# Kernel tuning notes

Measured on AMD Instinct MI355X. Metric: run time of the kernel, lower is better.

The kernel has to match this reference:

```python
import jax, jax.numpy as jnp
import numpy as np

N, E, IN, H, D = 50000, 800000, 128, 2, 64  # nodes, edges, in_dim, heads, out_dim per head
EPS = 1e-16  # PyG softmax denominator epsilon


def setup_inputs() -> dict:
    key = jax.random.key(0)
    ks = jax.random.split(key, 10)
    s = 1.0 / np.sqrt(IN)
    u = lambda k, shape: jax.random.uniform(k, shape, jnp.float32, -s, s)
    return {
        "x": jax.random.normal(ks[0], (N, IN), jnp.float32),
        "edge_index": jax.random.randint(ks[1], (2, E), 0, N, jnp.int64),
        "Wq": u(ks[2], (IN, H * D)), "bq": u(ks[3], (H * D,)),
        "Wk": u(ks[4], (IN, H * D)), "bk": u(ks[5], (H * D,)),
        "Wv": u(ks[6], (IN, H * D)), "bv": u(ks[7], (H * D,)),
        "Ws": u(ks[8], (IN, H * D)), "bs": u(ks[9], (H * D,)),
    }


def reference(x, edge_index, Wq, bq, Wk, bk, Wv, bv, Ws, bs):
    src, dst = edge_index[0], edge_index[1]
    # node-level projections [N, H, D]
    q = (x @ Wq + bq).reshape(N, H, D)
    k = (x @ Wk + bk).reshape(N, H, D)
    v = (x @ Wv + bv).reshape(N, H, D)
    # per-edge attention logits [E, H]
    alpha = jnp.einsum('ehd,ehd->eh', q[dst], k[src]) / np.float32(np.sqrt(D))
    # segment softmax over incoming edges of each dst node
    amax = jax.ops.segment_max(alpha, dst, num_segments=N)      # [N, H]
    amax = jnp.where(jnp.isfinite(amax), amax, 0.0)
    ealpha = jnp.exp(alpha - amax[dst])                          # [E, H]
    denom = jax.ops.segment_sum(ealpha, dst, num_segments=N)     # [N, H]
    w = ealpha / (denom[dst] + EPS)                              # [E, H]
    # scatter-aggregate weighted values -> [N, H, D]
    agg = jax.ops.segment_sum(w[:, :, None] * v[src], dst, num_segments=N)
    out = agg.reshape(N, H * D) + (x @ Ws + bs)                  # root/skip term
    return jax.nn.relu(out)
```

## Files before the change

kernel.cpp:

```cpp
#include <hip/hip_runtime.h>
#include <hip/hip_bf16.h>


#define N_NODES 50000
#define E_EDGES 800000
#define IN_DIM  128
#define HD      128
#define NPB     256
#define NB      196
#define EB      2048
#define NBLK_AC ((E_EDGES + EB - 1) / EB)
#define NTILES  ((N_NODES + 63) / 64)
#define PBLK    256
#define PSCALE  0.18033688011112042f

typedef float  f32x4  __attribute__((ext_vector_type(4)));
typedef float  f32x2  __attribute__((ext_vector_type(2)));
typedef __bf16 bf16x8 __attribute__((ext_vector_type(8)));
typedef unsigned short u16x8 __attribute__((ext_vector_type(8)));

__device__ __forceinline__ float bf2f(unsigned short u) {
    return __uint_as_float((unsigned int)u << 16);
}

__global__ __launch_bounds__(512) void proj_kernel(
    const float* __restrict__ x,
    const float* __restrict__ Wq, const float* __restrict__ bq,
    const float* __restrict__ Wk, const float* __restrict__ bk,
    const float* __restrict__ Wv, const float* __restrict__ bv,
    const float* __restrict__ Ws, const float* __restrict__ bs,
    __bf16* __restrict__ qb, unsigned char* __restrict__ kv8,
    __bf16* __restrict__ sbuf)
{
    __shared__ __bf16 xs[64][136];

    const int tid  = threadIdx.x;
    const int lane = tid & 63;
    const int wave = tid >> 6;
    const int l15  = lane & 15;
    const int g    = lane >> 4;

    const int p    = wave >> 1;
    const int colh = (wave & 1) * 64;
    const float* Wp     = (p == 0) ? Wq : (p == 1) ? Wk : (p == 2) ? Wv : Ws;
    const float* bias_p = (p == 0) ? bq : (p == 1) ? bk : (p == 2) ? bv : bs;

    bf16x8 Bf[4][4];
    #pragma unroll
    for (int ks = 0; ks < 4; ++ks) {
        #pragma unroll
        for (int cf = 0; cf < 4; ++cf) {
            bf16x8 b;
            #pragma unroll
            for (int j = 0; j < 8; ++j)
                b[j] = (__bf16)Wp[(size_t)(ks * 32 + g * 8 + j) * HD + colh + cf * 16 + l15];
            Bf[ks][cf] = b;
        }
    }

    float bias_v[4];
    #pragma unroll
    for (int cf = 0; cf < 4; ++cf) bias_v[cf] = bias_p[colh + cf * 16 + l15];

    const int srow = tid >> 5;
    const int sc4  = tid & 31;

    int t = blockIdx.x;
    float4 pre[4];
    if (t < NTILES) {
        #pragma unroll
        for (int it = 0; it < 4; ++it) {
            int row  = it * 16 + srow;
            int grow = t * 64 + row;
            pre[it] = (grow < N_NODES) ? *(const float4*)(x + (size_t)grow * IN_DIM + sc4 * 4)
                                       : make_float4(0.f, 0.f, 0.f, 0.f);
        }
    }

    for (; t < NTILES; t += PBLK) {
        __syncthreads();
        #pragma unroll
        for (int it = 0; it < 4; ++it) {
            int row = it * 16 + srow;
            __bf16* dst = &xs[row][sc4 * 4];
            dst[0] = (__bf16)pre[it].x; dst[1] = (__bf16)pre[it].y;
            dst[2] = (__bf16)pre[it].z; dst[3] = (__bf16)pre[it].w;
        }
        __syncthreads();

        int tn = t + PBLK;
        if (tn < NTILES) {
            #pragma unroll
            for (int it = 0; it < 4; ++it) {
                int row  = it * 16 + srow;
                int grow = tn * 64 + row;
                pre[it] = (grow < N_NODES) ? *(const float4*)(x + (size_t)grow * IN_DIM + sc4 * 4)
                                           : make_float4(0.f, 0.f, 0.f, 0.f);
            }
        }

        f32x4 acc[4][4];
        #pragma unroll
        for (int i = 0; i < 4; ++i)
            #pragma unroll
            for (int j = 0; j < 4; ++j) acc[i][j] = (f32x4){0.f, 0.f, 0.f, 0.f};

        #pragma unroll
        for (int ks = 0; ks < 4; ++ks) {
            #pragma unroll
            for (int rf = 0; rf < 4; ++rf) {
                bf16x8 A = *(const bf16x8*)&xs[rf * 16 + l15][ks * 32 + g * 8];
                #pragma unroll
                for (int cf = 0; cf < 4; ++cf)
                    acc[rf][cf] = __builtin_amdgcn_mfma_f32_16x16x32_bf16(A, Bf[ks][cf], acc[rf][cf], 0, 0, 0);
            }
        }

        const int nodebase = t * 64;
        if (p == 0 || p == 3) {
            __bf16* outp = (p == 0) ? qb : sbuf;
            #pragma unroll
            for (int cf = 0; cf < 4; ++cf) {
                int col = colh + cf * 16 + l15;
                #pragma unroll
                for (int rf = 0; rf < 4; ++rf) {
                    #pragma unroll
                    for (int r = 0; r < 4; ++r) {
                        int grow = nodebase + rf * 16 + g * 4 + r;
                        if (grow < N_NODES)
                            outp[(size_t)grow * HD + col] = (__bf16)(acc[rf][cf][r] + bias_v[cf]);
                    }
                }
            }
        } else {
            unsigned char* outp = kv8 + ((p == 2) ? 128 : 0);
            #pragma unroll
            for (int cf = 0; cf < 4; ++cf) {
                int col = colh + cf * 16 + l15;
                #pragma unroll
                for (int rf = 0; rf < 4; ++rf) {
                    #pragma unroll
                    for (int r = 0; r < 4; ++r) {
                        int grow = nodebase + rf * 16 + g * 4 + r;
                        if (grow < N_NODES) {
                            float val = acc[rf][cf][r] + bias_v[cf];
                            unsigned int pk = __builtin_amdgcn_cvt_pk_fp8_f32(val, val, 0, false);
                            outp[(size_t)grow * 256 + col] = (unsigned char)(pk & 0xff);
                        }
                    }
                }
            }
        }
    }
}

__global__ __launch_bounds__(256) void histA(
    const int* __restrict__ ei, int* __restrict__ hist)
{
    __shared__ int h[NB];
    const int tid = threadIdx.x;
    for (int i = tid; i < NB; i += 256) h[i] = 0;
    __syncthreads();

    const int* dsts = ei + E_EDGES;
    const int base = blockIdx.x * EB;
    #pragma unroll
    for (int half = 0; half < 2; ++half) {
        int e0 = base + half * 1024 + tid * 4;
        if (e0 + 3 < E_EDGES) {
            int4 d = *(const int4*)(dsts + e0);
            atomicAdd(&h[d.x >> 8], 1);
            atomicAdd(&h[d.y >> 8], 1);
            atomicAdd(&h[d.z >> 8], 1);
            atomicAdd(&h[d.w >> 8], 1);
        } else {
            for (int j = 0; j < 4; ++j)
                if (e0 + j < E_EDGES) atomicAdd(&h[dsts[e0 + j] >> 8], 1);
        }
    }
    __syncthreads();
    for (int i = tid; i < NB; i += 256)
        hist[i * NBLK_AC + blockIdx.x] = h[i];
}

__global__ __launch_bounds__(256) void scanB1(
    int* __restrict__ hist, int* __restrict__ sums)
{
    __shared__ int a[512];
    const int tid = threadIdx.x;
    const int b   = blockIdx.x;
    int* hb = hist + (size_t)b * NBLK_AC;

    a[tid]       = (tid       < NBLK_AC) ? hb[tid]       : 0;
    a[tid + 256] = (tid + 256 < NBLK_AC) ? hb[tid + 256] : 0;
    __syncthreads();
    #pragma unroll
    for (int d = 1; d < 512; d <<= 1) {
        int v0 = a[tid],       u0 = (tid       >= d) ? a[tid - d]       : 0;
        int v1 = a[tid + 256], u1 = (tid + 256 >= d) ? a[tid + 256 - d] : 0;
        __syncthreads();
        a[tid] = v0 + u0; a[tid + 256] = v1 + u1;
        __syncthreads();
    }
    if (tid < NBLK_AC)       hb[tid]       = (tid == 0) ? 0 : a[tid - 1];
    if (tid + 256 < NBLK_AC) hb[tid + 256] = a[tid + 255];
    if (tid == 0) sums[b] = a[NBLK_AC - 1];
}

__global__ __launch_bounds__(256) void scanB2(
    const int* __restrict__ sums, int* __restrict__ binbase)
{
    __shared__ int a[256];
    const int tid = threadIdx.x;
    a[tid] = (tid < NB) ? sums[tid] : 0;
    __syncthreads();
    #pragma unroll
    for (int d = 1; d < 256; d <<= 1) {
        int v = a[tid];
        int u = (tid >= d) ? a[tid - d] : 0;
        __syncthreads();
        a[tid] = v + u;
        __syncthreads();
    }
    if (tid < NB) binbase[tid] = (tid == 0) ? 0 : a[tid - 1];
    if (tid == 0) binbase[NB] = a[NB - 1] + 0;
    if (tid == 0) binbase[NB] = a[255];
}

__global__ __launch_bounds__(256) void scatterC(
    const int* __restrict__ ei, const int* __restrict__ hist,
    const int* __restrict__ binbase, int2* __restrict__ part)
{
    __shared__ int hb[NB];
    __shared__ int h2[NB];
    const int tid = threadIdx.x;
    for (int i = tid; i < NB; i += 256) {
        hb[i] = hist[i * NBLK_AC + blockIdx.x] + binbase[i];
        h2[i] = 0;
    }
    __syncthreads();

    const int* srcs = ei;
    const int* dsts = ei + E_EDGES;
    const int base = blockIdx.x * EB;
    #pragma unroll
    for (int half = 0; half < 2; ++half) {
        int e0 = base + half * 1024 + tid * 4;
        if (e0 + 3 < E_EDGES) {
            int4 s4 = *(const int4*)(srcs + e0);
            int4 d4 = *(const int4*)(dsts + e0);
            int bin, r;
            bin = d4.x >> 8; r = atomicAdd(&h2[bin], 1); part[hb[bin] + r] = make_int2(s4.x, d4.x);
            bin = d4.y >> 8; r = atomicAdd(&h2[bin], 1); part[hb[bin] + r] = make_int2(s4.y, d4.y);
            bin = d4.z >> 8; r = atomicAdd(&h2[bin], 1); part[hb[bin] + r] = make_int2(s4.z, d4.z);
            bin = d4.w >> 8; r = atomicAdd(&h2[bin], 1); part[hb[bin] + r] = make_int2(s4.w, d4.w);
        } else {
            for (int j = 0; j < 4; ++j) {
                if (e0 + j < E_EDGES) {
                    int sv = srcs[e0 + j], dv = dsts[e0 + j];
                    int bin = dv >> 8;
                    int r = atomicAdd(&h2[bin], 1);
                    part[hb[bin] + r] = make_int2(sv, dv);
                }
            }
        }
    }
}

__global__ __launch_bounds__(256) void buildD(
    const int2* __restrict__ part, const int* __restrict__ binbase,
    int* __restrict__ slot, int* __restrict__ nbase)
{
    __shared__ int cnt2[NPB];
    __shared__ int pfx[NPB];
    __shared__ int ofs[NPB];
    const int tid = threadIdx.x;
    const int b   = blockIdx.x;
    const int lo  = binbase[b];
    const int hi  = binbase[b + 1];
    const int n0  = b * NPB;

    cnt2[tid] = 0;
    __syncthreads();
    for (int i = lo + tid; i < hi; i += 256)
        atomicAdd(&cnt2[part[i].y - n0], 1);
    __syncthreads();

    pfx[tid] = cnt2[tid];
    __syncthreads();
    #pragma unroll
    for (int d = 1; d < NPB; d <<= 1) {
        int v = pfx[tid];
        int u = (tid >= d) ? pfx[tid - d] : 0;
        __syncthreads();
        pfx[tid] = v + u;
        __syncthreads();
    }
    const int excl = pfx[tid] - cnt2[tid];
    ofs[tid] = excl;
    const int node = n0 + tid;
    if (node < N_NODES) nbase[node] = lo + excl;
    if (b == NB - 1 && tid == 0) nbase[N_NODES] = E_EDGES;
    __syncthreads();

    for (int i = lo + tid; i < hi; i += 256) {
        int2 e = part[i];
        int r = atomicAdd(&ofs[e.y - n0], 1);
        slot[lo + r] = e.x;
    }
}

__global__ __launch_bounds__(256) void aggregate_kernel(
    const __bf16* __restrict__ qb, const unsigned char* __restrict__ kv8,
    const __bf16* __restrict__ sbuf,
    const int* __restrict__ nbase, const int* __restrict__ slot,
    float* __restrict__ out)
{
    const int tid  = threadIdx.x;
    const int lane = tid & 63;
    const int wave = tid >> 6;
    const int h    = lane >> 5;
    const int lh   = lane & 31;
    const int s    = lh >> 4;
    const int l16  = lh & 15;
    const int node = blockIdx.x * 8 + wave * 2 + h;
    const bool nvalid = node < N_NODES;
    const int nc = nvalid ? node : 0;

    const int bse = nbase[nc];
    const int deg = nvalid ? (nbase[nc + 1] - bse) : 0;

    u16x8 qu = *(const u16x8*)(qb + (size_t)nc * HD + 8 * l16);
    float qf[8];
    #pragma unroll
    for (int c = 0; c < 8; ++c) qf[c] = bf2f(qu[c]);

    int my_src = (lh < deg) ? slot[bse + lh] : 0;

    float lsum = 0.f;
    float acc[8];
    #pragma unroll
    for (int c = 0; c < 8; ++c) acc[c] = 0.f;

    const int sbase = h * 32;
    for (int i = 0; i < deg; i += 8) {
        int  jj[4], se[4];
        uint2 kr[4], vr[4];
        float d[4];

        #pragma unroll
        for (int r = 0; r < 4; ++r) {
            jj[r] = i + 2 * r + s;
            int sv = __shfl(my_src, sbase + (jj[r] & 31), 64);
            if (jj[r] >= 32) sv = slot[bse + jj[r]];
            se[r] = (jj[r] < deg) ? sv : 0;
        }
        #pragma unroll
        for (int r = 0; r < 4; ++r) {
            const unsigned char* rowp = kv8 + (size_t)se[r] * 256 + 8 * l16;
            kr[r] = *(const uint2*)rowp;
            vr[r] = *(const uint2*)(rowp + 128);
        }
        #pragma unroll
        for (int r = 0; r < 4; ++r) {
            f32x2 ka = __builtin_amdgcn_cvt_pk_f32_fp8(kr[r].x, 0);
            f32x2 kb_ = __builtin_amdgcn_cvt_pk_f32_fp8(kr[r].x, 1);
            f32x2 kc = __builtin_amdgcn_cvt_pk_f32_fp8(kr[r].y, 0);
            f32x2 kd = __builtin_amdgcn_cvt_pk_f32_fp8(kr[r].y, 1);
            d[r] = qf[0] * ka.x + qf[1] * ka.y + qf[2] * kb_.x + qf[3] * kb_.y
                 + qf[4] * kc.x + qf[5] * kc.y + qf[6] * kd.x + qf[7] * kd.y;
        }
        #pragma unroll
        for (int m = 1; m <= 4; m <<= 1) {
            d[0] += __shfl_xor(d[0], m);
            d[1] += __shfl_xor(d[1], m);
            d[2] += __shfl_xor(d[2], m);
            d[3] += __shfl_xor(d[3], m);
        }
        #pragma unroll
        for (int r = 0; r < 4; ++r) {
            float a2 = (jj[r] < deg) ? d[r] * PSCALE : -INFINITY;
            float p  = exp2f(a2);
            lsum += p;
            f32x2 va = __builtin_amdgcn_cvt_pk_f32_fp8(vr[r].x, 0);
            f32x2 vb_ = __builtin_amdgcn_cvt_pk_f32_fp8(vr[r].x, 1);
            f32x2 vc = __builtin_amdgcn_cvt_pk_f32_fp8(vr[r].y, 0);
            f32x2 vd = __builtin_amdgcn_cvt_pk_f32_fp8(vr[r].y, 1);
            acc[0] += p * va.x;  acc[1] += p * va.y;
            acc[2] += p * vb_.x; acc[3] += p * vb_.y;
            acc[4] += p * vc.x;  acc[5] += p * vc.y;
            acc[6] += p * vd.x;  acc[7] += p * vd.y;
        }
    }

    lsum += __shfl_xor(lsum, 16);
    #pragma unroll
    for (int c = 0; c < 8; ++c) acc[c] += __shfl_xor(acc[c], 16);

    float inv = (deg > 0) ? 1.f / (lsum + 1e-16f) : 0.f;
    u16x8 su = *(const u16x8*)(sbuf + (size_t)nc * HD + 8 * l16);

    f32x4 ov;
    #pragma unroll
    for (int cc = 0; cc < 4; ++cc) {
        float av;
        unsigned short sv;
        switch (cc) {
            case 0: av = s ? acc[4] : acc[0]; sv = s ? su[4] : su[0]; break;
            case 1: av = s ? acc[5] : acc[1]; sv = s ? su[5] : su[1]; break;
            case 2: av = s ? acc[6] : acc[2]; sv = s ? su[6] : su[2]; break;
            default: av = s ? acc[7] : acc[3]; sv = s ? su[7] : su[3]; break;
        }
        ov[cc] = fmaxf(av * inv + bf2f(sv), 0.f);
    }
    if (nvalid)
        *(f32x4*)(out + (size_t)node * HD + 8 * l16 + 4 * s) = ov;
}

extern "C" void kernel_launch(void* const* d_in, const int* in_sizes, int n_in,
                              void* d_out, int out_size, void* d_ws, size_t ws_size,
                              hipStream_t stream)
{
    const float* x  = (const float*)d_in[0];
    const int*   ei = (const int*)d_in[1];
    const float* Wq = (const float*)d_in[2];
    const float* bq = (const float*)d_in[3];
    const float* Wk = (const float*)d_in[4];
    const float* bk = (const float*)d_in[5];
    const float* Wv = (const float*)d_in[6];
    const float* bv = (const float*)d_in[7];
    const float* Ws = (const float*)d_in[8];
    const float* bs = (const float*)d_in[9];

    char* ws = (char*)d_ws;
    size_t off = 0;
    auto alloc = [&](size_t bytes) {
        void* p = ws + off;
        off += (bytes + 255) & ~(size_t)255;
        return p;
    };
    const size_t projB = (size_t)N_NODES * HD * sizeof(__bf16);
    __bf16* qb = (__bf16*)alloc(projB);
    unsigned char* kv8 = (unsigned char*)alloc((size_t)N_NODES * 256);
    __bf16* sbf = (__bf16*)alloc(projB);
    int* hist    = (int*)alloc((size_t)NB * NBLK_AC * sizeof(int));
    int* sums    = (int*)alloc((size_t)NB * sizeof(int));
    int* binbase = (int*)alloc((size_t)(NB + 1) * sizeof(int));
    int2* part   = (int2*)alloc((size_t)E_EDGES * sizeof(int2));
    int* slot    = (int*)alloc((size_t)E_EDGES * sizeof(int));
    int* nbase   = (int*)alloc((size_t)(N_NODES + 1) * sizeof(int));

    histA<<<NBLK_AC, 256, 0, stream>>>(ei, hist);
    scanB1<<<NB, 256, 0, stream>>>(hist, sums);
    scanB2<<<1, 256, 0, stream>>>(sums, binbase);
    scatterC<<<NBLK_AC, 256, 0, stream>>>(ei, hist, binbase, part);
    buildD<<<NB, 256, 0, stream>>>(part, binbase, slot, nbase);

    proj_kernel<<<PBLK, 512, 0, stream>>>(
        x, Wq, bq, Wk, bk, Wv, bv, Ws, bs, qb, kv8, sbf);

    aggregate_kernel<<<(N_NODES + 7) / 8, 256, 0, stream>>>(
        qb, kv8, sbf, nbase, slot, (float*)d_out);
}
```

Measured before the change: 91.97 us.

## Fuse partition kernels into one cooperative kernel and widen aggregate unroll

Merges the five CSR-building kernels (histogram, two scans, scatter, per-bin build) into a single cooperative launch that uses grid-wide syncs between phases, so four kernel launches and their gaps go away. The aggregate loop now processes 16 edges per iteration instead of 8, putting more gathers in flight. The projection grid is doubled from 256 to 512 blocks. The trade-offs are grid.sync overhead, the requirement that all 391 blocks be co-resident, and higher register pressure in the aggregate kernel.

```diff
diff --git a/kernel.cpp b/kernel.cpp
--- a/kernel.cpp
+++ b/kernel.cpp
@@ -1,5 +1,6 @@
 #include <hip/hip_runtime.h>
 #include <hip/hip_bf16.h>
+#include <hip/hip_cooperative_groups.h>
 
 
 #define N_NODES 50000
@@ -11,7 +12,7 @@
 #define EB      2048
 #define NBLK_AC ((E_EDGES + EB - 1) / EB)
 #define NTILES  ((N_NODES + 63) / 64)
-#define PBLK    256
+#define PBLK    512
 #define PSCALE  0.18033688011112042f
 
 typedef float  f32x4  __attribute__((ext_vector_type(4)));
@@ -154,159 +155,145 @@
     }
 }
 
-__global__ __launch_bounds__(256) void histA(
-    const int* __restrict__ ei, int* __restrict__ hist)
+__global__ __launch_bounds__(256) void partition_coop(
+    const int* __restrict__ ei, int* __restrict__ hist, int* __restrict__ sums,
+    int* __restrict__ binbase, int2* __restrict__ part,
+    int* __restrict__ slot, int* __restrict__ nbase)
 {
-    __shared__ int h[NB];
+    namespace cg = cooperative_groups;
+    cg::grid_group grid = cg::this_grid();
+    __shared__ int sh[768];
     const int tid = threadIdx.x;
-    for (int i = tid; i < NB; i += 256) h[i] = 0;
+    const int blk = blockIdx.x;
+    const int base = blk * EB;
+    const int* srcs = ei;
+    const int* dsts = ei + E_EDGES;
+
+    for (int i = tid; i < NB; i += 256) sh[i] = 0;
     __syncthreads();
-
-    const int* dsts = ei + E_EDGES;
-    const int base = blockIdx.x * EB;
     #pragma unroll
     for (int half = 0; half < 2; ++half) {
         int e0 = base + half * 1024 + tid * 4;
         if (e0 + 3 < E_EDGES) {
             int4 d = *(const int4*)(dsts + e0);
-            atomicAdd(&h[d.x >> 8], 1);
-            atomicAdd(&h[d.y >> 8], 1);
-            atomicAdd(&h[d.z >> 8], 1);
-            atomicAdd(&h[d.w >> 8], 1);
+            atomicAdd(&sh[d.x >> 8], 1);
+            atomicAdd(&sh[d.y >> 8], 1);
+            atomicAdd(&sh[d.z >> 8], 1);
+            atomicAdd(&sh[d.w >> 8], 1);
         } else {
             for (int j = 0; j < 4; ++j)
-                if (e0 + j < E_EDGES) atomicAdd(&h[dsts[e0 + j] >> 8], 1);
+                if (e0 + j < E_EDGES) atomicAdd(&sh[dsts[e0 + j] >> 8], 1);
         }
     }
     __syncthreads();
     for (int i = tid; i < NB; i += 256)
-        hist[i * NBLK_AC + blockIdx.x] = h[i];
-}
-
-__global__ __launch_bounds__(256) void scanB1(
-    int* __restrict__ hist, int* __restrict__ sums)
-{
-    __shared__ int a[512];
-    const int tid = threadIdx.x;
-    const int b   = blockIdx.x;
-    int* hb = hist + (size_t)b * NBLK_AC;
-
-    a[tid]       = (tid       < NBLK_AC) ? hb[tid]       : 0;
-    a[tid + 256] = (tid + 256 < NBLK_AC) ? hb[tid + 256] : 0;
-    __syncthreads();
-    #pragma unroll
-    for (int d = 1; d < 512; d <<= 1) {
-        int v0 = a[tid],       u0 = (tid       >= d) ? a[tid - d]       : 0;
-        int v1 = a[tid + 256], u1 = (tid + 256 >= d) ? a[tid + 256 - d] : 0;
-        __syncthreads();
-        a[tid] = v0 + u0; a[tid + 256] = v1 + u1;
-        __syncthreads();
-    }
-    if (tid < NBLK_AC)       hb[tid]       = (tid == 0) ? 0 : a[tid - 1];
-    if (tid + 256 < NBLK_AC) hb[tid + 256] = a[tid + 255];
-    if (tid == 0) sums[b] = a[NBLK_AC - 1];
-}
-
-__global__ __launch_bounds__(256) void scanB2(
-    const int* __restrict__ sums, int* __restrict__ binbase)
-{
-    __shared__ int a[256];
-    const int tid = threadIdx.x;
-    a[tid] = (tid < NB) ? sums[tid] : 0;
-    __syncthreads();
-    #pragma unroll
-    for (int d = 1; d < 256; d <<= 1) {
-        int v = a[tid];
-        int u = (tid >= d) ? a[tid - d] : 0;
-        __syncthreads();
-        a[tid] = v + u;
-        __syncthreads();
-    }
-    if (tid < NB) binbase[tid] = (tid == 0) ? 0 : a[tid - 1];
-    if (tid == 0) binbase[NB] = a[NB - 1] + 0;
-    if (tid == 0) binbase[NB] = a[255];
-}
-
-__global__ __launch_bounds__(256) void scatterC(
-    const int* __restrict__ ei, const int* __restrict__ hist,
-    const int* __restrict__ binbase, int2* __restrict__ part)
-{
-    __shared__ int hb[NB];
-    __shared__ int h2[NB];
-    const int tid = threadIdx.x;
-    for (int i = tid; i < NB; i += 256) {
-        hb[i] = hist[i * NBLK_AC + blockIdx.x] + binbase[i];
-        h2[i] = 0;
-    }
-    __syncthreads();
-
-    const int* srcs = ei;
-    const int* dsts = ei + E_EDGES;
-    const int base = blockIdx.x * EB;
-    #pragma unroll
-    for (int half = 0; half < 2; ++half) {
-        int e0 = base + half * 1024 + tid * 4;
-        if (e0 + 3 < E_EDGES) {
-            int4 s4 = *(const int4*)(srcs + e0);
-            int4 d4 = *(const int4*)(dsts + e0);
-            int bin, r;
-            bin = d4.x >> 8; r = atomicAdd(&h2[bin], 1); part[hb[bin] + r] = make_int2(s4.x, d4.x);
-            bin = d4.y >> 8; r = atomicAdd(&h2[bin], 1); part[hb[bin] + r] = make_int2(s4.y, d4.y);
-            bin = d4.z >> 8; r = atomicAdd(&h2[bin], 1); part[hb[bin] + r] = make_int2(s4.z, d4.z);
-            bin = d4.w >> 8; r = atomicAdd(&h2[bin], 1); part[hb[bin] + r] = make_int2(s4.w, d4.w);
-        } else {
-            for (int j = 0; j < 4; ++j) {
-                if (e0 + j < E_EDGES) {
-                    int sv = srcs[e0 + j], dv = dsts[e0 + j];
-                    int bin = dv >> 8;
-                    int r = atomicAdd(&h2[bin], 1);
-                    part[hb[bin] + r] = make_int2(sv, dv);
+        hist[i * NBLK_AC + blk] = sh[i];
+    grid.sync();
+
+    if (blk < NB) {
+        int* hb = hist + (size_t)blk * NBLK_AC;
+        sh[tid]       = (tid       < NBLK_AC) ? hb[tid]       : 0;
+        sh[tid + 256] = (tid + 256 < NBLK_AC) ? hb[tid + 256] : 0;
+        __syncthreads();
+        #pragma unroll
+        for (int d = 1; d < 512; d <<= 1) {
+            int v0 = sh[tid],       u0 = (tid       >= d) ? sh[tid - d]       : 0;
+            int v1 = sh[tid + 256], u1 = (tid + 256 >= d) ? sh[tid + 256 - d] : 0;
+            __syncthreads();
+            sh[tid] = v0 + u0; sh[tid + 256] = v1 + u1;
+            __syncthreads();
+        }
+        if (tid < NBLK_AC)       hb[tid]       = (tid == 0) ? 0 : sh[tid - 1];
+        if (tid + 256 < NBLK_AC) hb[tid + 256] = sh[tid + 255];
+        if (tid == 0) sums[blk] = sh[NBLK_AC - 1];
+    }
+    grid.sync();
+
+    if (blk == 0) {
+        sh[tid] = (tid < NB) ? sums[tid] : 0;
+        __syncthreads();
+        #pragma unroll
+        for (int d = 1; d < 256; d <<= 1) {
+            int v = sh[tid];
+            int u = (tid >= d) ? sh[tid - d] : 0;
+            __syncthreads();
+            sh[tid] = v + u;
+            __syncthreads();
+        }
+        if (tid < NB) binbase[tid] = (tid == 0) ? 0 : sh[tid - 1];
+        if (tid == 0) binbase[NB] = sh[255];
+    }
+    grid.sync();
+
+    {
+        int* hb2 = sh;
+        int* h2  = sh + 256;
+        for (int i = tid; i < NB; i += 256) {
+            hb2[i] = hist[i * NBLK_AC + blk] + binbase[i];
+            h2[i]  = 0;
+        }
+        __syncthreads();
+        #pragma unroll
+        for (int half = 0; half < 2; ++half) {
+            int e0 = base + half * 1024 + tid * 4;
+            if (e0 + 3 < E_EDGES) {
+                int4 s4 = *(const int4*)(srcs + e0);
+                int4 d4 = *(const int4*)(dsts + e0);
+                int bin, r;
+                bin = d4.x >> 8; r = atomicAdd(&h2[bin], 1); part[hb2[bin] + r] = make_int2(s4.x, d4.x);
+                bin = d4.y >> 8; r = atomicAdd(&h2[bin], 1); part[hb2[bin] + r] = make_int2(s4.y, d4.y);
+                bin = d4.z >> 8; r = atomicAdd(&h2[bin], 1); part[hb2[bin] + r] = make_int2(s4.z, d4.z);
+                bin = d4.w >> 8; r = atomicAdd(&h2[bin], 1); part[hb2[bin] + r] = make_int2(s4.w, d4.w);
+            } else {
+                for (int j = 0; j < 4; ++j) {
+                    if (e0 + j < E_EDGES) {
+                        int sv = srcs[e0 + j], dv = dsts[e0 + j];
+                        int bin = dv >> 8;
+                        int r = atomicAdd(&h2[bin], 1);
+                        part[hb2[bin] + r] = make_int2(sv, dv);
+                    }
                 }
             }
         }
     }
-}
-
-__global__ __launch_bounds__(256) void buildD(
-    const int2* __restrict__ part, const int* __restrict__ binbase,
-    int* __restrict__ slot, int* __restrict__ nbase)
-{
-    __shared__ int cnt2[NPB];
-    __shared__ int pfx[NPB];
-    __shared__ int ofs[NPB];
-    const int tid = threadIdx.x;
-    const int b   = blockIdx.x;
-    const int lo  = binbase[b];
-    const int hi  = binbase[b + 1];
-    const int n0  = b * NPB;
-
-    cnt2[tid] = 0;
-    __syncthreads();
-    for (int i = lo + tid; i < hi; i += 256)
-        atomicAdd(&cnt2[part[i].y - n0], 1);
-    __syncthreads();
-
-    pfx[tid] = cnt2[tid];
-    __syncthreads();
-    #pragma unroll
-    for (int d = 1; d < NPB; d <<= 1) {
-        int v = pfx[tid];
-        int u = (tid >= d) ? pfx[tid - d] : 0;
-        __syncthreads();
-        pfx[tid] = v + u;
-        __syncthreads();
-    }
-    const int excl = pfx[tid] - cnt2[tid];
-    ofs[tid] = excl;
-    const int node = n0 + tid;
-    if (node < N_NODES) nbase[node] = lo + excl;
-    if (b == NB - 1 && tid == 0) nbase[N_NODES] = E_EDGES;
-    __syncthreads();
-
-    for (int i = lo + tid; i < hi; i += 256) {
-        int2 e = part[i];
-        int r = atomicAdd(&ofs[e.y - n0], 1);
-        slot[lo + r] = e.x;
+    grid.sync();
+
+    if (blk < NB) {
+        int* cnt2 = sh;
+        int* pfx  = sh + 256;
+        int* ofs  = sh + 512;
+        const int lo = binbase[blk];
+        const int hi = binbase[blk + 1];
+        const int n0 = blk * NPB;
+
+        cnt2[tid] = 0;
+        __syncthreads();
+        for (int i = lo + tid; i < hi; i += 256)
+            atomicAdd(&cnt2[part[i].y - n0], 1);
+        __syncthreads();
+
+        pfx[tid] = cnt2[tid];
+        __syncthreads();
+        #pragma unroll
+        for (int d = 1; d < NPB; d <<= 1) {
+            int v = pfx[tid];
+            int u = (tid >= d) ? pfx[tid - d] : 0;
+            __syncthreads();
+            pfx[tid] = v + u;
+            __syncthreads();
+        }
+        const int excl = pfx[tid] - cnt2[tid];
+        ofs[tid] = excl;
+        const int node = n0 + tid;
+        if (node < N_NODES) nbase[node] = lo + excl;
+        if (blk == NB - 1 && tid == 0) nbase[N_NODES] = E_EDGES;
+        __syncthreads();
+
+        for (int i = lo + tid; i < hi; i += 256) {
+            int2 e = part[i];
+            int r = atomicAdd(&ofs[e.y - n0], 1);
+            slot[lo + r] = e.x;
+        }
     }
 }
 
@@ -343,26 +330,26 @@
     for (int c = 0; c < 8; ++c) acc[c] = 0.f;
 
     const int sbase = h * 32;
-    for (int i = 0; i < deg; i += 8) {
-        int  jj[4], se[4];
-        uint2 kr[4], vr[4];
-        float d[4];
-
-        #pragma unroll
-        for (int r = 0; r < 4; ++r) {
+    for (int i = 0; i < deg; i += 16) {
+        int  jj[8], se[8];
+        uint2 kr[8], vr[8];
+        float d[8];
+
+        #pragma unroll
+        for (int r = 0; r < 8; ++r) {
             jj[r] = i + 2 * r + s;
             int sv = __shfl(my_src, sbase + (jj[r] & 31), 64);
             if (jj[r] >= 32) sv = slot[bse + jj[r]];
             se[r] = (jj[r] < deg) ? sv : 0;
         }
         #pragma unroll
-        for (int r = 0; r < 4; ++r) {
+        for (int r = 0; r < 8; ++r) {
             const unsigned char* rowp = kv8 + (size_t)se[r] * 256 + 8 * l16;
             kr[r] = *(const uint2*)rowp;
             vr[r] = *(const uint2*)(rowp + 128);
         }
         #pragma unroll
-        for (int r = 0; r < 4; ++r) {
+        for (int r = 0; r < 8; ++r) {
             f32x2 ka = __builtin_amdgcn_cvt_pk_f32_fp8(kr[r].x, 0);
             f32x2 kb_ = __builtin_amdgcn_cvt_pk_f32_fp8(kr[r].x, 1);
             f32x2 kc = __builtin_amdgcn_cvt_pk_f32_fp8(kr[r].y, 0);
@@ -372,13 +359,12 @@
         }
         #pragma unroll
         for (int m = 1; m <= 4; m <<= 1) {
-            d[0] += __shfl_xor(d[0], m);
-            d[1] += __shfl_xor(d[1], m);
-            d[2] += __shfl_xor(d[2], m);
-            d[3] += __shfl_xor(d[3], m);
-        }
-        #pragma unroll
-        for (int r = 0; r < 4; ++r) {
+            #pragma unroll
+            for (int r = 0; r < 8; ++r)
+                d[r] += __shfl_xor(d[r], m);
+        }
+        #pragma unroll
+        for (int r = 0; r < 8; ++r) {
             float a2 = (jj[r] < deg) ? d[r] * PSCALE : -INFINITY;
             float p  = exp2f(a2);
             lsum += p;
@@ -450,11 +436,10 @@
     int* slot    = (int*)alloc((size_t)E_EDGES * sizeof(int));
     int* nbase   = (int*)alloc((size_t)(N_NODES + 1) * sizeof(int));
 
-    histA<<<NBLK_AC, 256, 0, stream>>>(ei, hist);
-    scanB1<<<NB, 256, 0, stream>>>(hist, sums);
-    scanB2<<<1, 256, 0, stream>>>(sums, binbase);
-    scatterC<<<NBLK_AC, 256, 0, stream>>>(ei, hist, binbase, part);
-    buildD<<<NB, 256, 0, stream>>>(part, binbase, slot, nbase);
+    void* cargs[] = { (void*)&ei, (void*)&hist, (void*)&sums, (void*)&binbase,
+                      (void*)&part, (void*)&slot, (void*)&nbase };
+    hipLaunchCooperativeKernel((void*)partition_coop, dim3(NBLK_AC), dim3(256),
+                               cargs, 0, stream);
 
     proj_kernel<<<PBLK, 512, 0, stream>>>(
         x, Wq, bq, Wk, bk, Wv, bv, Ws, bs, qb, kv8, sbf);
```

Result: slower. 287.8 us (+212.9%).
